# Optimization experiments

Hardware: AMD Instinct MI355X
Metric: run time of the kernel (lower is better)

## Reference

```python
import jax, jax.numpy as jnp
import numpy as np

B, C_IN, C_OUT, H, K = 64, 64, 128, 1855, 6


def setup_inputs() -> dict:
    key = jax.random.key(0)
    k1, k2, k3, k4 = jax.random.split(key, 4)
    x = jax.random.normal(k1, (B, C_IN, H), dtype=jnp.float32)
    # neighbor table [H, K]; valid indices first, -1 padding at the end
    neighbors = jax.random.randint(k2, (H, K), 0, H)
    n_boundary = H // 10
    neighbors = neighbors.at[:n_boundary, K - 2:].set(-1)
    weight_center = jax.random.normal(k3, (C_OUT, C_IN), dtype=jnp.float32) / np.sqrt(C_IN).astype(np.float32)
    weight_neighbors = jax.random.normal(k4, (C_OUT, C_IN, K), dtype=jnp.float32) / np.sqrt(C_IN * K).astype(np.float32)
    bias = jnp.zeros((C_OUT,), dtype=jnp.float32)
    return {
        "x": x,
        "neighbors": neighbors,
        "weight_center": weight_center,
        "weight_neighbors": weight_neighbors,
        "bias": bias,
    }


def reference(x, neighbors, weight_center, weight_neighbors, bias):
    # x: [B, C_in, H]; neighbors: [H, K] with -1 = invalid (valid-first ordering)
    mask = neighbors >= 0                               # [H, K]
    idx = jnp.where(mask, neighbors, 0)                 # safe gather indices
    gathered = x[:, :, idx] * mask.astype(x.dtype)[None, None, :, :]  # [B, C_in, H, K]
    center = jnp.einsum('bch,oc->boh', x, weight_center)              # [B, C_out, H]
    neigh = jnp.einsum('bchk,ock->boh', gathered, weight_neighbors)   # [B, C_out, H]
    counts = (1 + mask.sum(axis=-1)).astype(x.dtype)                  # [H]
    return (center + neigh) / counts[None, None, :] + bias[None, :, None]
```

## Files before the change

kernel.cpp:

```cpp
#include <hip/hip_runtime.h>
#include <stdint.h>

typedef __bf16 bf16x8 __attribute__((ext_vector_type(8)));
typedef float floatx4 __attribute__((ext_vector_type(4)));
typedef unsigned int u32x4 __attribute__((ext_vector_type(4)));
typedef unsigned short u16;
typedef unsigned int u32;

#define CIN   64
#define COUT  128
#define H_    1855
#define KNB   6
#define KTOT  448
#define NSTEPS 14
#define RS    456

#define PIN4(v) asm volatile("" : "+v"(v))

static __device__ inline u16 f32_to_bf16(float f) {
    u32 u = __float_as_uint(f);
    u32 r = (u + 0x7FFFu + ((u >> 16) & 1u)) >> 16;
    return (u16)r;
}

__global__ __launch_bounds__(256) void k_transpose(const float* __restrict__ x,
                                                   u16* __restrict__ xt3) {
    __shared__ u16 tile[64][65];
    int h0  = blockIdx.x * 64;
    int bc0 = blockIdx.y * 64;
    int lane = threadIdx.x & 63;
    int rowq = threadIdx.x >> 6;
    int h = h0 + lane;
    bool hv = h < H_;
#pragma unroll
    for (int i = 0; i < 16; ++i) {
        int row = i * 4 + rowq;
        u16 v = 0;
        if (hv) v = f32_to_bf16(x[(size_t)(bc0 + row) * H_ + h]);
        tile[row][lane] = v;
    }
    __syncthreads();
#pragma unroll
    for (int i = 0; i < 16; ++i) {
        int hr = i * 4 + rowq;
        int hh = h0 + hr;
        if (hh < H_) xt3[(size_t)hh * 4096 + bc0 + lane] = tile[lane][hr];
    }
}

__global__ __launch_bounds__(256) void k_pack(const float* __restrict__ wc,
                                              const float* __restrict__ wn,
                                              const int* __restrict__ nbr,
                                              u16* __restrict__ wp,
                                              float* __restrict__ cInvG) {
    int tg = blockIdx.x * 256 + threadIdx.x;
    if (tg < H_) {
        int cnt = 1;
#pragma unroll
        for (int j = 0; j < KNB; ++j) cnt += (nbr[tg * KNB + j] >= 0) ? 1 : 0;
        cInvG[tg] = 1.0f / (float)cnt;
    }
    if (tg >= COUT * KTOT) return;
    int o = tg / KTOT;
    int rem = tg - o * KTOT;
    int s = rem >> 6, c = rem & 63;
    float v = (s == 0) ? wc[o * CIN + c]
                       : wn[(o * CIN + c) * KNB + (s - 1)];
    wp[tg] = f32_to_bf16(v);
}

__global__ __launch_bounds__(256, 2) void k_main(const u16* __restrict__ xt3,
                                                 const u16* __restrict__ wp,
                                                 const int* __restrict__ nbr,
                                                 const float* __restrict__ bias,
                                                 const float* __restrict__ cInvG,
                                                 float* __restrict__ out) {
    __shared__ __align__(16) u16 X[29248];

    int tid  = threadIdx.x;
    int g    = blockIdx.x;
    int bp   = g & 31;
    int T    = g >> 5;
    int b0   = bp * 2;

    int lane = tid & 63;
    int wave = tid >> 6;
    int col  = lane & 15;
    int quad = lane >> 4;
    int m0w  = wave * 32;
    int blg  = (lane >> 3) & 1;
    int chunk = lane & 7;

    u32x4 afrag[2][NSTEPS];
#pragma unroll
    for (int mt = 0; mt < 2; ++mt) {
        int o = m0w + mt * 16 + col;
#pragma unroll
        for (int kk = 0; kk < NSTEPS; ++kk)
            afrag[mt][kk] = *(const u32x4*)(wp + o * KTOT + kk * 32 + quad * 8);
    }
#pragma unroll
    for (int mt = 0; mt < 2; ++mt)
#pragma unroll
        for (int kk = 0; kk < NSTEPS; ++kk)
            PIN4(afrag[mt][kk]);

    float biasv[2][4];
#pragma unroll
    for (int mt = 0; mt < 2; ++mt)
#pragma unroll
        for (int r = 0; r < 4; ++r)
            biasv[mt][r] = bias[m0w + mt * 16 + quad * 4 + r];

#pragma unroll
    for (int tt = 0; tt < 2; ++tt) {
        int t = T * 2 + tt;
        int h0 = t * 32;
        __syncthreads();

#pragma unroll
        for (int i = 0; i < 14; ++i) {
            int hl = wave * 8 + (i < 7 ? 0 : 4) + quad;
            int s  = (i < 7) ? i : (i - 7);
            int h  = h0 + hl;
            int src = -1;
            if (h < H_) src = (s == 0) ? h : nbr[h * KNB + (s - 1)];
            u32x4 v = (u32x4){0u, 0u, 0u, 0u};
            if (src >= 0)
                v = *(const u32x4*)(xt3 + (size_t)src * 4096 + (b0 + blg) * 64 + chunk * 8);
            int n = blg * 32 + hl;
            *(u32x4*)(X + n * RS + (n >> 3) * 8 + s * 64 + chunk * 8) = v;
        }
        __syncthreads();

        int hA = h0 + col, hB = h0 + 16 + col;
        float icA = cInvG[hA < H_ ? hA : 0];
        float icB = cInvG[hB < H_ ? hB : 0];

        floatx4 acc[2][4];
#pragma unroll
        for (int mt = 0; mt < 2; ++mt)
#pragma unroll
            for (int nt = 0; nt < 4; ++nt)
                acc[mt][nt] = (floatx4){0.0f, 0.0f, 0.0f, 0.0f};

        int rb[4];
#pragma unroll
        for (int nt = 0; nt < 4; ++nt) {
            int n = nt * 16 + col;
            rb[nt] = n * RS + (n >> 3) * 8 + quad * 8;
        }

#pragma unroll
        for (int kk = 0; kk < NSTEPS; ++kk) {
            bf16x8 a0 = __builtin_bit_cast(bf16x8, afrag[0][kk]);
            bf16x8 a1 = __builtin_bit_cast(bf16x8, afrag[1][kk]);
#pragma unroll
            for (int nt = 0; nt < 4; ++nt) {
                bf16x8 bfr = *(const bf16x8*)(X + rb[nt] + kk * 32);
                acc[0][nt] = __builtin_amdgcn_mfma_f32_16x16x32_bf16(
                    a0, bfr, acc[0][nt], 0, 0, 0);
                acc[1][nt] = __builtin_amdgcn_mfma_f32_16x16x32_bf16(
                    a1, bfr, acc[1][nt], 0, 0, 0);
            }
        }

        __syncthreads();

        float* stage = (float*)X;
#pragma unroll
        for (int mt = 0; mt < 2; ++mt)
#pragma unroll
            for (int nt = 0; nt < 4; ++nt) {
                float ic = (nt & 1) ? icB : icA;
                int n = nt * 16 + col;
#pragma unroll
                for (int r = 0; r < 4; ++r) {
                    int o = m0w + mt * 16 + quad * 4 + r;
                    stage[o * 66 + n] = acc[mt][nt][r] * ic + biasv[mt][r];
                }
            }

        int hl2 = lane & 31, bl2 = lane >> 5;
        int hh = h0 + hl2;
        bool hv = hh < H_;
#pragma unroll
        for (int rr = 0; rr < 32; ++rr) {
            int o = m0w + rr;
            if (hv)
                out[((size_t)(b0 + bl2) * COUT + o) * H_ + hh] = stage[o * 66 + lane];
        }
    }
}

extern "C" void kernel_launch(void* const* d_in, const int* in_sizes, int n_in,
                              void* d_out, int out_size, void* d_ws, size_t ws_size,
                              hipStream_t stream) {
    const float* x    = (const float*)d_in[0];
    const int*   nbr  = (const int*)d_in[1];
    const float* wc   = (const float*)d_in[2];
    const float* wn   = (const float*)d_in[3];
    const float* bias = (const float*)d_in[4];

    u16*   xt3   = (u16*)d_ws;
    u16*   wp    = (u16*)((char*)d_ws + (size_t)H_ * 4096 * 2);
    float* cInvG = (float*)((char*)d_ws + (size_t)H_ * 4096 * 2 + (size_t)COUT * KTOT * 2);

    k_pack<<<dim3((COUT * KTOT) / 256), dim3(256), 0, stream>>>(wc, wn, nbr, wp, cInvG);
    k_transpose<<<dim3(29, 64), dim3(256), 0, stream>>>(x, xt3);
    k_main<<<dim3(928), dim3(256), 0, stream>>>(xt3, wp, nbr, bias, cInvG, (float*)d_out);
}
```

Before: 153.2 us.

## Double-buffer neighbor gather via direct global-to-LDS loads with smaller h-tiles

```diff
diff --git a/kernel.cpp b/kernel.cpp
--- a/kernel.cpp
+++ b/kernel.cpp
@@ -13,9 +13,22 @@
 #define KNB   6
 #define KTOT  448
 #define NSTEPS 14
-#define RS    456
+
+#define HLROW 2064
+#define BUFSZ 33024
+#define STCP  36
+
+#define WP_OFF   ((size_t)H_ * 4096 * 2)
+#define CINV_OFF (WP_OFF + (size_t)COUT * KTOT * 2)
+#define ZERO_OFF (CINV_OFF + 7424)
 
 #define PIN4(v) asm volatile("" : "+v"(v))
+
+typedef __attribute__((address_space(1))) unsigned int as1_u32;
+typedef __attribute__((address_space(3))) unsigned int as3_u32;
+static __device__ __forceinline__ void ld16_to_lds(const void* g, void* l) {
+    __builtin_amdgcn_global_load_lds((const as1_u32*)g, (as3_u32*)l, 16, 0, 0);
+}
 
 static __device__ inline u16 f32_to_bf16(float f) {
     u32 u = __float_as_uint(f);
@@ -52,8 +65,10 @@
                                               const float* __restrict__ wn,
                                               const int* __restrict__ nbr,
                                               u16* __restrict__ wp,
-                                              float* __restrict__ cInvG) {
+                                              float* __restrict__ cInvG,
+                                              u32* __restrict__ zeroPg) {
     int tg = blockIdx.x * 256 + threadIdx.x;
+    if (tg < 64) zeroPg[tg] = 0u;
     if (tg < H_) {
         int cnt = 1;
 #pragma unroll
@@ -69,27 +84,54 @@
     wp[tg] = f32_to_bf16(v);
 }
 
+static __device__ __forceinline__ void stage_tile(
+    const u16* __restrict__ xt3, const int* __restrict__ nbr,
+    const char* __restrict__ zeroPg, char* bufB,
+    int h0t, int b0, int wave, int lane) {
+    int lane16 = lane & 15;
+    int ssub   = lane >> 4;
+    int bl     = lane16 >> 3;
+    int chunk  = lane16 & 7;
+#pragma unroll
+    for (int i = 0; i < 8; ++i) {
+        int hlL = i & 3;
+        int sg  = i >> 2;
+        int hl  = wave * 4 + hlL;
+        int s   = sg * 4 + ssub;
+        int hh  = h0t + hl;
+        int hcl = hh < H_ ? hh : 0;
+        int sidx = (s >= 1 && s <= 6) ? (s - 1) : 0;
+        int nv  = nbr[hcl * KNB + sidx];
+        int src = (s == 0) ? hcl : nv;
+        bool valid = (hh < H_) && (s <= 6) && (src >= 0);
+        const char* gp = valid
+            ? (const char*)(xt3 + (size_t)src * 4096 + (b0 + bl) * 64 + chunk * 8)
+            : (zeroPg + lane16 * 16);
+        ld16_to_lds(gp, bufB + hl * HLROW + sg * 1024);
+    }
+}
+
 __global__ __launch_bounds__(256, 2) void k_main(const u16* __restrict__ xt3,
                                                  const u16* __restrict__ wp,
                                                  const int* __restrict__ nbr,
                                                  const float* __restrict__ bias,
                                                  const float* __restrict__ cInvG,
+                                                 const char* __restrict__ zeroPg,
                                                  float* __restrict__ out) {
-    __shared__ __align__(16) u16 X[29248];
+    __shared__ __align__(16) char LDS[2 * BUFSZ];
 
     int tid  = threadIdx.x;
     int g    = blockIdx.x;
     int bp   = g & 31;
-    int T    = g >> 5;
+    int hs   = g >> 5;
     int b0   = bp * 2;
+    int h0   = hs * 64;
 
     int lane = tid & 63;
     int wave = tid >> 6;
     int col  = lane & 15;
     int quad = lane >> 4;
     int m0w  = wave * 32;
-    int blg  = (lane >> 3) & 1;
-    int chunk = lane & 7;
 
     u32x4 afrag[2][NSTEPS];
 #pragma unroll
@@ -112,83 +154,65 @@
         for (int r = 0; r < 4; ++r)
             biasv[mt][r] = bias[m0w + mt * 16 + quad * 4 + r];
 
-#pragma unroll
-    for (int tt = 0; tt < 2; ++tt) {
-        int t = T * 2 + tt;
-        int h0 = t * 32;
+    int rb0 = col * HLROW + quad * 16;
+    int rb1 = rb0 + 128;
+
+    stage_tile(xt3, nbr, zeroPg, LDS, h0, b0, wave, lane);
+
+#pragma unroll
+    for (int tt = 0; tt < 4; ++tt) {
+        int h0t = h0 + tt * 16;
+        char* cur = LDS + (tt & 1) * BUFSZ;
+
         __syncthreads();
 
-#pragma unroll
-        for (int i = 0; i < 14; ++i) {
-            int hl = wave * 8 + (i < 7 ? 0 : 4) + quad;
-            int s  = (i < 7) ? i : (i - 7);
-            int h  = h0 + hl;
-            int src = -1;
-            if (h < H_) src = (s == 0) ? h : nbr[h * KNB + (s - 1)];
-            u32x4 v = (u32x4){0u, 0u, 0u, 0u};
-            if (src >= 0)
-                v = *(const u32x4*)(xt3 + (size_t)src * 4096 + (b0 + blg) * 64 + chunk * 8);
-            int n = blg * 32 + hl;
-            *(u32x4*)(X + n * RS + (n >> 3) * 8 + s * 64 + chunk * 8) = v;
-        }
-        __syncthreads();
-
-        int hA = h0 + col, hB = h0 + 16 + col;
-        float icA = cInvG[hA < H_ ? hA : 0];
-        float icB = cInvG[hB < H_ ? hB : 0];
-
-        floatx4 acc[2][4];
+        if (tt < 3)
+            stage_tile(xt3, nbr, zeroPg, LDS + ((tt + 1) & 1) * BUFSZ,
+                       h0t + 16, b0, wave, lane);
+
+        floatx4 acc[2][2];
 #pragma unroll
         for (int mt = 0; mt < 2; ++mt)
 #pragma unroll
-            for (int nt = 0; nt < 4; ++nt)
+            for (int nt = 0; nt < 2; ++nt)
                 acc[mt][nt] = (floatx4){0.0f, 0.0f, 0.0f, 0.0f};
 
-        int rb[4];
-#pragma unroll
-        for (int nt = 0; nt < 4; ++nt) {
-            int n = nt * 16 + col;
-            rb[nt] = n * RS + (n >> 3) * 8 + quad * 8;
-        }
-
 #pragma unroll
         for (int kk = 0; kk < NSTEPS; ++kk) {
+            int koff = (kk >> 1) * 256 + (kk & 1) * 64;
+            bf16x8 bf0 = *(const bf16x8*)(cur + rb0 + koff);
+            bf16x8 bf1 = *(const bf16x8*)(cur + rb1 + koff);
             bf16x8 a0 = __builtin_bit_cast(bf16x8, afrag[0][kk]);
             bf16x8 a1 = __builtin_bit_cast(bf16x8, afrag[1][kk]);
-#pragma unroll
-            for (int nt = 0; nt < 4; ++nt) {
-                bf16x8 bfr = *(const bf16x8*)(X + rb[nt] + kk * 32);
-                acc[0][nt] = __builtin_amdgcn_mfma_f32_16x16x32_bf16(
-                    a0, bfr, acc[0][nt], 0, 0, 0);
-                acc[1][nt] = __builtin_amdgcn_mfma_f32_16x16x32_bf16(
-                    a1, bfr, acc[1][nt], 0, 0, 0);
-            }
+            acc[0][0] = __builtin_amdgcn_mfma_f32_16x16x32_bf16(a0, bf0, acc[0][0], 0, 0, 0);
+            acc[1][0] = __builtin_amdgcn_mfma_f32_16x16x32_bf16(a1, bf0, acc[1][0], 0, 0, 0);
+            acc[0][1] = __builtin_amdgcn_mfma_f32_16x16x32_bf16(a0, bf1, acc[0][1], 0, 0, 0);
+            acc[1][1] = __builtin_amdgcn_mfma_f32_16x16x32_bf16(a1, bf1, acc[1][1], 0, 0, 0);
         }
 
         __syncthreads();
 
-        float* stage = (float*)X;
+        float* stC = (float*)cur;
+        int hEp = h0t + col;
+        float ic = cInvG[hEp < H_ ? hEp : 0];
 #pragma unroll
         for (int mt = 0; mt < 2; ++mt)
 #pragma unroll
-            for (int nt = 0; nt < 4; ++nt) {
-                float ic = (nt & 1) ? icB : icA;
-                int n = nt * 16 + col;
+            for (int nt = 0; nt < 2; ++nt)
 #pragma unroll
                 for (int r = 0; r < 4; ++r) {
                     int o = m0w + mt * 16 + quad * 4 + r;
-                    stage[o * 66 + n] = acc[mt][nt][r] * ic + biasv[mt][r];
+                    stC[o * STCP + nt * 16 + col] = acc[mt][nt][r] * ic + biasv[mt][r];
                 }
-            }
-
-        int hl2 = lane & 31, bl2 = lane >> 5;
-        int hh = h0 + hl2;
-        bool hv = hh < H_;
-#pragma unroll
-        for (int rr = 0; rr < 32; ++rr) {
-            int o = m0w + rr;
-            if (hv)
-                out[((size_t)(b0 + bl2) * COUT + o) * H_ + hh] = stage[o * 66 + lane];
+        int n5 = lane & 31, q2 = lane >> 5;
+        int colS = n5 & 15, ntS = n5 >> 4;
+        int hS = h0t + colS;
+        bool hv = hS < H_;
+        size_t obase = ((size_t)(b0 + ntS) * COUT) * H_ + hS;
+#pragma unroll
+        for (int rr = 0; rr < 16; ++rr) {
+            int o = m0w + rr * 2 + q2;
+            if (hv) out[obase + (size_t)o * H_] = stC[o * STCP + n5];
         }
     }
 }
@@ -202,11 +226,14 @@
     const float* wn   = (const float*)d_in[3];
     const float* bias = (const float*)d_in[4];
 
-    u16*   xt3   = (u16*)d_ws;
-    u16*   wp    = (u16*)((char*)d_ws + (size_t)H_ * 4096 * 2);
-    float* cInvG = (float*)((char*)d_ws + (size_t)H_ * 4096 * 2 + (size_t)COUT * KTOT * 2);
-
-    k_pack<<<dim3((COUT * KTOT) / 256), dim3(256), 0, stream>>>(wc, wn, nbr, wp, cInvG);
+    u16*   xt3    = (u16*)d_ws;
+    u16*   wp     = (u16*)((char*)d_ws + WP_OFF);
+    float* cInvG  = (float*)((char*)d_ws + CINV_OFF);
+    u32*   zeroPg = (u32*)((char*)d_ws + ZERO_OFF);
+
+    k_pack<<<dim3((COUT * KTOT + 255) / 256), dim3(256), 0, stream>>>(
+        wc, wn, nbr, wp, cInvG, zeroPg);
     k_transpose<<<dim3(29, 64), dim3(256), 0, stream>>>(x, xt3);
-    k_main<<<dim3(928), dim3(256), 0, stream>>>(xt3, wp, nbr, bias, cInvG, (float*)d_out);
-}
+    k_main<<<dim3(928), dim3(256), 0, stream>>>(
+        xt3, wp, nbr, bias, cInvG, (const char*)zeroPg, (float*)d_out);
+}
```

Result: faster. 139.1 us (-9.2%).
